# Kernel tuning notes

Measured on AMD Instinct MI355X. Metric: run time of the kernel, lower is better.

## Reference

```python
import jax, jax.numpy as jnp
import numpy as np
from jax import lax

DIM = 512


def rmsnorm(x, gamma):
    # F.normalize(x, dim=-1) * sqrt(dim) * (gamma + 1)
    n = jnp.maximum(jnp.linalg.norm(x, axis=-1, keepdims=True), 1e-12)
    return x / n * (DIM ** 0.5) * (gamma + 1.0)


def lru_layer(x, Wn, Wif, Whf, bhf):
    # x: [b, t, d]. Precompute the input-dependent projections as big matmuls,
    # then scan the genuinely sequential hidden recurrence.
    nh = jnp.tanh(jnp.einsum('btd,de->bte', x, Wn))   # candidate hidden
    ifg = jnp.einsum('btd,de->bte', x, Wif)            # input forget logits
    b = x.shape[0]
    h0 = jnp.zeros((b, DIM), dtype=x.dtype)            # init_hidden buffer (zeros)

    def step(h, inp):
        nh_t, if_t = inp                               # [b, d] each
        g = jax.nn.sigmoid(h @ Whf + bhf + if_t)       # forget gate
        h_next = h + g * (nh_t - h)                    # lerp(h, nh, g)
        return h_next, h_next

    _, hs = lax.scan(step, h0, (jnp.swapaxes(nh, 0, 1), jnp.swapaxes(ifg, 0, 1)))
    return jnp.swapaxes(hs, 0, 1)                      # [b, t, d]


def gate_cell(x, hidden, Wn, Wif, Whf, bhf):
    # LightRecurrentUnitCell applied pointwise over [b, t, d] with hidden=x_in
    nh = jnp.tanh(jnp.einsum('btd,de->bte', x, Wn))
    g = jax.nn.sigmoid(jnp.einsum('btd,de->bte', hidden, Whf) + bhf
                       + jnp.einsum('btd,de->bte', x, Wif))
    return hidden + g * (nh - hidden)


def setup_inputs() -> dict:
    key = jax.random.key(0)
    ks = jax.random.split(key, 12)
    s = 1.0 / np.sqrt(DIM)
    def w(k):
        return jax.random.uniform(k, (DIM, DIM), jnp.float32, -s, s)
    inp = {
        'x': jax.random.normal(ks[0], (32, 2048, DIM), jnp.float32),
        'gamma': jnp.zeros((DIM,), jnp.float32),
        'g_Wn': w(ks[1]), 'g_Wif': w(ks[2]), 'g_Whf': w(ks[3]),
        'g_bhf': jax.random.uniform(ks[4], (DIM,), jnp.float32, -s, s),
        'l0_Wn': w(ks[5]), 'l0_Wif': w(ks[6]), 'l0_Whf': w(ks[7]),
        'l0_bhf': jax.random.uniform(ks[8], (DIM,), jnp.float32, -s, s),
        'l1_Wn': w(ks[9]), 'l1_Wif': w(ks[10]), 'l1_Whf': w(ks[11]),
        'l1_bhf': jax.random.uniform(jax.random.fold_in(key, 99), (DIM,), jnp.float32, -s, s),
    }
    return inp


def reference(x, gamma, g_Wn, g_Wif, g_Whf, g_bhf,
              l0_Wn, l0_Wif, l0_Whf, l0_bhf,
              l1_Wn, l1_Wif, l1_Whf, l1_bhf):
    xn = rmsnorm(x, gamma)
    h = lru_layer(xn, l0_Wn, l0_Wif, l0_Whf, l0_bhf)
    h = lru_layer(h, l1_Wn, l1_Wif, l1_Whf, l1_bhf)
    lru_out = gate_cell(h, xn, g_Wn, g_Wif, g_Whf, g_bhf)
    return lru_out + x
```

## Files before the change

### kernel.cpp

```cpp
#include <hip/hip_runtime.h>
#include <stdint.h>

#define D 512
#define BATCH 32
#define TT 2048
#define BT (BATCH*TT)

typedef unsigned short u16;
typedef __attribute__((ext_vector_type(8))) short bf16x8;
typedef __attribute__((ext_vector_type(4))) float f32x4;

__device__ __forceinline__ float bf2f(u16 u){
  union { unsigned int i; float f; } v; v.i = ((unsigned int)u) << 16; return v.f;
}
__device__ __forceinline__ u16 f2bf(float f){
  union { float f; unsigned int i; } v; v.f = f;
  unsigned int r = (v.i + 0x7fffu + ((v.i >> 16) & 1u)) >> 16;
  return (u16)r;
}

__device__ __forceinline__ int dot4i8(int a, int b, int c){
#if __has_builtin(__builtin_amdgcn_sdot4)
  return __builtin_amdgcn_sdot4(a, b, c, false);
#else
  c += (int)(char)(a      ) * (int)(char)(b      );
  c += (int)(char)(a >>  8) * (int)(char)(b >>  8);
  c += (int)(char)(a >> 16) * (int)(char)(b >> 16);
  c += (int)(char)(a >> 24) * (int)(char)(b >> 24);
  return c;
#endif
}

__global__ __launch_bounds__(256) void rmsnorm_k(const float* __restrict__ x,
                                                 const float* __restrict__ gamma,
                                                 u16* __restrict__ xn){
  int row = blockIdx.x;
  int t = threadIdx.x;
  const float* xr = x + (size_t)row * D;
  float v0 = xr[t];
  float v1 = xr[t + 256];
  float s = v0*v0 + v1*v1;
  #pragma unroll
  for (int o = 32; o > 0; o >>= 1) s += __shfl_down(s, o);
  __shared__ float red[4];
  int lane = t & 63, wv = t >> 6;
  if (lane == 0) red[wv] = s;
  __syncthreads();
  float tot = red[0] + red[1] + red[2] + red[3];
  float n = fmaxf(sqrtf(tot), 1e-12f);
  float sc = 22.627416997969522f / n;
  u16* o_ = xn + (size_t)row * D;
  o_[t]       = f2bf(v0 * sc * (gamma[t] + 1.f));
  o_[t + 256] = f2bf(v1 * sc * (gamma[t + 256] + 1.f));
}

__global__ __launch_bounds__(256) void transpose_k(const float* __restrict__ src,
                                                   u16* __restrict__ dst){
  __shared__ u16 tile[32][33];
  int bx = blockIdx.x * 32, by = blockIdx.y * 32;
  int tx = threadIdx.x & 31, ty = threadIdx.x >> 5;
  #pragma unroll
  for (int i = 0; i < 32; i += 8)
    tile[ty + i][tx] = f2bf(src[(size_t)(by + ty + i) * D + bx + tx]);
  __syncthreads();
  #pragma unroll
  for (int i = 0; i < 32; i += 8)
    dst[(size_t)(bx + ty + i) * D + by + tx] = tile[tx][ty + i];
}

__global__ __launch_bounds__(64) void quant_col_k(const float* __restrict__ W,
                                                  int* __restrict__ Wq,
                                                  float* __restrict__ sc){
  int e = blockIdx.x;
  int lane = threadIdx.x;
  float w[8];
  float m = 0.f;
  #pragma unroll
  for (int j = 0; j < 8; j++){
    w[j] = W[(size_t)(lane*8 + j) * D + e];
    m = fmaxf(m, fabsf(w[j]));
  }
  #pragma unroll
  for (int o = 32; o > 0; o >>= 1) m = fmaxf(m, __shfl_xor(m, o));
  float inv = (m > 0.f) ? (127.f / m) : 0.f;
  int q[8];
  #pragma unroll
  for (int j = 0; j < 8; j++){
    int v = __float2int_rn(w[j] * inv);
    v = v < -127 ? -127 : (v > 127 ? 127 : v);
    q[j] = v & 0xff;
  }
  int p0 = q[0] | (q[1] << 8) | (q[2] << 16) | (q[3] << 24);
  int p1 = q[4] | (q[5] << 8) | (q[6] << 16) | (q[7] << 24);
  Wq[e*128 + lane*2]     = p0;
  Wq[e*128 + lane*2 + 1] = p1;
  if (lane == 0) sc[e] = m / (127.f * 127.f);
}

__global__ __launch_bounds__(256) void gemm_bt_k(const u16* __restrict__ A,
                                                 const u16* __restrict__ Bt,
                                                 u16* __restrict__ C,
                                                 int do_tanh){
  __shared__ __align__(16) u16 As[128*32];
  __shared__ __align__(16) u16 Bs[128*32];
  int tid = threadIdx.x;
  int bm = blockIdx.x, bn = blockIdx.y;
  int wv = tid >> 6, lane = tid & 63;
  int wm = (wv & 1) * 64, wn = (wv >> 1) * 64;
  int m0 = lane & 15, quad = lane >> 4;
  f32x4 acc[4][4];
  #pragma unroll
  for (int i = 0; i < 4; i++)
    #pragma unroll
    for (int j = 0; j < 4; j++){
      f32x4 z = {0.f, 0.f, 0.f, 0.f};
      acc[i][j] = z;
    }
  const size_t arow = (size_t)bm * 128;
  const size_t brow = (size_t)bn * 128;
  for (int k0 = 0; k0 < D; k0 += 32){
    __syncthreads();
    #pragma unroll
    for (int i = 0; i < 2; i++){
      int c = tid + 256*i;
      int r = c >> 2, ko = (c & 3) * 8;
      ((int4*)As)[c] = *(const int4*)(A  + (arow + r) * D + k0 + ko);
      ((int4*)Bs)[c] = *(const int4*)(Bt + (brow + r) * D + k0 + ko);
    }
    __syncthreads();
    bf16x8 af[4], bfr[4];
    #pragma unroll
    for (int i = 0; i < 4; i++){
      af[i]  = *(const bf16x8*)(As + (wm + i*16 + m0) * 32 + quad*8);
      bfr[i] = *(const bf16x8*)(Bs + (wn + i*16 + m0) * 32 + quad*8);
    }
    #pragma unroll
    for (int i = 0; i < 4; i++)
      #pragma unroll
      for (int j = 0; j < 4; j++)
        acc[i][j] = __builtin_amdgcn_mfma_f32_16x16x32_bf16(af[i], bfr[j], acc[i][j], 0, 0, 0);
  }
  #pragma unroll
  for (int i = 0; i < 4; i++)
    #pragma unroll
    for (int j = 0; j < 4; j++)
      #pragma unroll
      for (int r = 0; r < 4; r++){
        size_t row = arow + wm + i*16 + quad*4 + r;
        int col = bn*128 + wn + j*16 + m0;
        float v = acc[i][j][r];
        if (do_tanh) v = tanhf(v);
        C[row * D + col] = f2bf(v);
      }
}

__global__ __launch_bounds__(512, 2) void lru_scan_k(u16* __restrict__ Nn,
                                                     const u16* __restrict__ Ff,
                                                     const int* __restrict__ Wq,
                                                     const float* __restrict__ sc,
                                                     const float* __restrict__ bhf){
  int tid = threadIdx.x;
  int b = blockIdx.x;
  int wv = tid >> 6, l = tid & 63;
  int m  = l & 15;
  int q2 = l >> 4;
  int base_e = wv*64 + m*4;
  int e = base_e + q2;

  int4 wq[4][8];
  #pragma unroll
  for (int j = 0; j < 4; j++){
    const int* wp = Wq + (size_t)(base_e + j) * 128 + q2*32;
    #pragma unroll
    for (int i = 0; i < 8; i++) wq[j][i] = ((const int4*)wp)[i];
  }
  float scale = sc[e];
  float bias  = bhf[e];

  __shared__ __align__(16) char hq[2][512];
  if (tid < 128) ((int*)hq[0])[tid] = 0;
  float h = 0.f;
  const size_t base = (size_t)b * TT * D + e;
  u16* np = Nn + base;
  const u16* fp = Ff + base;
  float nv  = bf2f(np[0]);
  float fvb = bf2f(fp[0]) + bias;
  __syncthreads();

  for (int t = 0; t < TT; t++){
    float nv_n = 0.f, fvb_n = 0.f;
    if (t < TT - 1){
      nv_n  = bf2f(np[(size_t)(t+1) * D]);
      fvb_n = bf2f(fp[(size_t)(t+1) * D]) + bias;
    }
    const char* hb = hq[t & 1] + q2*128;
    int p0 = 0, p1 = 0, p2 = 0, p3 = 0;
    #pragma unroll
    for (int i = 0; i < 8; i++){
      int4 a = ((const int4*)hb)[i];
      p0 = dot4i8(wq[0][i].x, a.x, p0); p0 = dot4i8(wq[0][i].y, a.y, p0);
      p0 = dot4i8(wq[0][i].z, a.z, p0); p0 = dot4i8(wq[0][i].w, a.w, p0);
      p1 = dot4i8(wq[1][i].x, a.x, p1); p1 = dot4i8(wq[1][i].y, a.y, p1);
      p1 = dot4i8(wq[1][i].z, a.z, p1); p1 = dot4i8(wq[1][i].w, a.w, p1);
      p2 = dot4i8(wq[2][i].x, a.x, p2); p2 = dot4i8(wq[2][i].y, a.y, p2);
      p2 = dot4i8(wq[2][i].z, a.z, p2); p2 = dot4i8(wq[2][i].w, a.w, p2);
      p3 = dot4i8(wq[3][i].x, a.x, p3); p3 = dot4i8(wq[3][i].y, a.y, p3);
      p3 = dot4i8(wq[3][i].z, a.z, p3); p3 = dot4i8(wq[3][i].w, a.w, p3);
    }
    int b0 = q2 & 1, b1 = q2 >> 1;
    int send0 = b0 ? p0 : p1, keep0 = b0 ? p1 : p0;
    int send1 = b0 ? p2 : p3, keep1 = b0 ? p3 : p2;
    int z0 = keep0 + __shfl_xor(send0, 16);
    int z1 = keep1 + __shfl_xor(send1, 16);
    int zs = b1 ? z0 : z1, zk = b1 ? z1 : z0;
    int z  = zk + __shfl_xor(zs, 32);
    float arg = (float)z * scale + fvb;
    float g = 1.f / (1.f + __expf(-arg));
    h = h + g * (nv - h);
    np[(size_t)t * D] = f2bf(h);
    int q = __float2int_rn(h * 127.f);
    q = q < -127 ? -127 : (q > 127 ? 127 : q);
    hq[(t+1) & 1][e] = (char)q;
    nv = nv_n; fvb = fvb_n;
    asm volatile("s_waitcnt lgkmcnt(0)\n\ts_barrier" ::: "memory");
  }
}

__global__ __launch_bounds__(256) void final1_k(const u16* __restrict__ xn,
                                                u16* __restrict__ Nng,
                                                const u16* __restrict__ Ffg,
                                                const u16* __restrict__ Ghf,
                                                const float* __restrict__ gbhf){
  size_t i = (size_t)blockIdx.x * 256 + threadIdx.x;
  int e = (int)(i & (D - 1));
  float xnv = bf2f(xn[i]);
  float nv  = bf2f(Nng[i]);
  float arg = bf2f(Ghf[i]) + gbhf[e] + bf2f(Ffg[i]);
  float g = 1.f / (1.f + __expf(-arg));
  float lru = xnv + g * (nv - xnv);
  Nng[i] = f2bf(lru);
}

__global__ __launch_bounds__(256) void final2_k(const u16* __restrict__ lru,
                                                const float* __restrict__ x,
                                                float* __restrict__ out){
  size_t i = (size_t)blockIdx.x * 256 + threadIdx.x;
  out[i] = bf2f(lru[i]) + x[i];
}

extern "C" void kernel_launch(void* const* d_in, const int* in_sizes, int n_in,
                              void* d_out, int out_size, void* d_ws, size_t ws_size,
                              hipStream_t stream){
  const float* x      = (const float*)d_in[0];
  const float* gamma  = (const float*)d_in[1];
  const float* g_Wn   = (const float*)d_in[2];
  const float* g_Wif  = (const float*)d_in[3];
  const float* g_Whf  = (const float*)d_in[4];
  const float* g_bhf  = (const float*)d_in[5];
  const float* l0_Wn  = (const float*)d_in[6];
  const float* l0_Wif = (const float*)d_in[7];
  const float* l0_Whf = (const float*)d_in[8];
  const float* l0_bhf = (const float*)d_in[9];
  const float* l1_Wn  = (const float*)d_in[10];
  const float* l1_Wif = (const float*)d_in[11];
  const float* l1_Whf = (const float*)d_in[12];
  const float* l1_bhf = (const float*)d_in[13];
  float* out = (float*)d_out;

  char* ws = (char*)d_ws;
  const size_t PLANE = (size_t)BT * D * 2;
  u16* P0 = (u16*)(ws);
  u16* P1 = (u16*)(ws + PLANE);
  u16* P2 = (u16*)d_out;
  u16* P3 = P2 + (size_t)BT * D;

  char* wb = ws + 2*PLANE;
  const size_t WSZ = (size_t)D * D * 2;
  u16* T_l0Wn  = (u16*)(wb + 0*WSZ);
  u16* T_l0Wif = (u16*)(wb + 1*WSZ);
  u16* T_gWhf  = (u16*)(wb + 2*WSZ);
  u16* T_l1Wn  = (u16*)(wb + 3*WSZ);
  u16* T_l1Wif = (u16*)(wb + 4*WSZ);
  u16* T_gWn   = (u16*)(wb + 5*WSZ);
  u16* T_gWif  = (u16*)(wb + 6*WSZ);
  int*   Wq0 = (int*)  (wb + 7*WSZ);
  int*   Wq1 = (int*)  (wb + 7*WSZ + (size_t)D*D);
  float* sc0 = (float*)(wb + 7*WSZ + 2*(size_t)D*D);
  float* sc1 = (float*)(wb + 7*WSZ + 2*(size_t)D*D + D*4);

  dim3 tb(256), tg(16, 16);
  transpose_k<<<tg, tb, 0, stream>>>(l0_Wn,  T_l0Wn);
  transpose_k<<<tg, tb, 0, stream>>>(l0_Wif, T_l0Wif);
  transpose_k<<<tg, tb, 0, stream>>>(g_Whf,  T_gWhf);
  transpose_k<<<tg, tb, 0, stream>>>(l1_Wn,  T_l1Wn);
  transpose_k<<<tg, tb, 0, stream>>>(l1_Wif, T_l1Wif);
  transpose_k<<<tg, tb, 0, stream>>>(g_Wn,   T_gWn);
  transpose_k<<<tg, tb, 0, stream>>>(g_Wif,  T_gWif);
  quant_col_k<<<512, 64, 0, stream>>>(l0_Whf, Wq0, sc0);
  quant_col_k<<<512, 64, 0, stream>>>(l1_Whf, Wq1, sc1);

  rmsnorm_k<<<BT, 256, 0, stream>>>(x, gamma, P0);

  dim3 gg(BT/128, D/128);
  gemm_bt_k<<<gg, tb, 0, stream>>>(P0, T_l0Wn,  P1, 1);
  gemm_bt_k<<<gg, tb, 0, stream>>>(P0, T_l0Wif, P2, 0);
  lru_scan_k<<<BATCH, 512, 0, stream>>>(P1, P2, Wq0, sc0, l0_bhf);
  gemm_bt_k<<<gg, tb, 0, stream>>>(P1, T_l1Wn,  P3, 1);
  gemm_bt_k<<<gg, tb, 0, stream>>>(P1, T_l1Wif, P2, 0);
  lru_scan_k<<<BATCH, 512, 0, stream>>>(P3, P2, Wq1, sc1, l1_bhf);
  gemm_bt_k<<<gg, tb, 0, stream>>>(P3, T_gWn,  P1, 1);
  gemm_bt_k<<<gg, tb, 0, stream>>>(P3, T_gWif, P2, 0);
  gemm_bt_k<<<gg, tb, 0, stream>>>(P0, T_gWhf, P3, 0);

  final1_k<<<BT*D/256, 256, 0, stream>>>(P0, P1, P2, P3, g_bhf);
  final2_k<<<BT*D/256, 256, 0, stream>>>(P1, x, out);
}
```

Measured before the change: 4.195 ms.

## Fuse both LRU scans and middle GEMMs into one pipelined persistent kernel

Replaces the layer-0 scan, the two layer-1 projection GEMMs and the layer-1 scan with one 96-block kernel. Blocks 0-31 run the layer-0 scan and publish progress flags every 64 timesteps. Blocks 32-63 compute the layer-1 projections per 64-row chunk as soon as it is ready, and blocks 64-95 run the layer-1 scan behind them. The goal is to overlap the two sequential scans and the GEMM so the second scan no longer waits for the first to finish. In exchange it relies on all 96 blocks being co-resident, since it spin-waits on flags with a bounded timeout. The projection blocks also read weights straight from global memory with less reuse than the tiled GEMM.

```diff
diff --git a/kernel.cpp b/kernel.cpp
--- a/kernel.cpp
+++ b/kernel.cpp
@@ -29,6 +29,15 @@
   c += (int)(char)(a >> 24) * (int)(char)(b >> 24);
   return c;
 #endif
+}
+
+__device__ __forceinline__ void spin_wait_ge(const int* p, int target){
+  int iters = 0;
+  while (__hip_atomic_load(p, __ATOMIC_RELAXED, __HIP_MEMORY_SCOPE_AGENT) < target){
+    __builtin_amdgcn_s_sleep(16);
+    if (++iters > 4000000) break;
+  }
+  __builtin_amdgcn_fence(__ATOMIC_ACQUIRE, "agent");
 }
 
 __global__ __launch_bounds__(256) void rmsnorm_k(const float* __restrict__ x,
@@ -154,13 +163,13 @@
       }
 }
 
-__global__ __launch_bounds__(512, 2) void lru_scan_k(u16* __restrict__ Nn,
-                                                     const u16* __restrict__ Ff,
-                                                     const int* __restrict__ Wq,
-                                                     const float* __restrict__ sc,
-                                                     const float* __restrict__ bhf){
-  int tid = threadIdx.x;
-  int b = blockIdx.x;
+__device__ __forceinline__ void scan_core(u16* __restrict__ Nn,
+                                          const u16* __restrict__ Ff,
+                                          const int* __restrict__ Wq,
+                                          const float* __restrict__ sc,
+                                          const float* __restrict__ bhf,
+                                          int b, int tid, char* smem,
+                                          int* prog_pub, const int* prog_wait){
   int wv = tid >> 6, l = tid & 63;
   int m  = l & 15;
   int q2 = l >> 4;
@@ -177,17 +186,23 @@
   float scale = sc[e];
   float bias  = bhf[e];
 
-  __shared__ __align__(16) char hq[2][512];
-  if (tid < 128) ((int*)hq[0])[tid] = 0;
+  char (*hq)[512] = (char(*)[512])smem;
+  if (tid < 128) ((int*)smem)[tid] = 0;
   float h = 0.f;
   const size_t base = (size_t)b * TT * D + e;
   u16* np = Nn + base;
   const u16* fp = Ff + base;
+
+  if (prog_wait) spin_wait_ge(prog_wait + b, 128);
   float nv  = bf2f(np[0]);
   float fvb = bf2f(fp[0]) + bias;
   __syncthreads();
 
   for (int t = 0; t < TT; t++){
+    if (prog_wait && t && (t & 63) == 0){
+      int target = t + 128; if (target > TT) target = TT;
+      spin_wait_ge(prog_wait + b, target);
+    }
     float nv_n = 0.f, fvb_n = 0.f;
     if (t < TT - 1){
       nv_n  = bf2f(np[(size_t)(t+1) * D]);
@@ -223,7 +238,106 @@
     hq[(t+1) & 1][e] = (char)q;
     nv = nv_n; fvb = fvb_n;
     asm volatile("s_waitcnt lgkmcnt(0)\n\ts_barrier" ::: "memory");
-  }
+    if (prog_pub && (t & 63) == 63){
+      asm volatile("s_waitcnt vmcnt(0)" ::: "memory");
+      __syncthreads();
+      if (tid == 0)
+        __hip_atomic_store(prog_pub + b, t + 1, __ATOMIC_RELEASE,
+                           __HIP_MEMORY_SCOPE_AGENT);
+    }
+  }
+}
+
+#define LDA 260
+__global__ __launch_bounds__(512, 1) void fused_mid_k(
+    u16* __restrict__ P1,
+    const u16* __restrict__ P2,
+    u16* __restrict__ P3,
+    const u16* __restrict__ Wn1t, const u16* __restrict__ Wif1t,
+    const int* __restrict__ Wq0, const float* __restrict__ sc0,
+    const float* __restrict__ bhf0,
+    const int* __restrict__ Wq1, const float* __restrict__ sc1,
+    const float* __restrict__ bhf1,
+    int* __restrict__ prog0, int* __restrict__ prog1){
+  __shared__ __align__(16) char smem[64 * LDA * 2];
+  int blk = blockIdx.x, tid = threadIdx.x;
+
+  if (blk < 32){
+    scan_core(P1, P2, Wq0, sc0, bhf0, blk, tid, smem, prog0, nullptr);
+  } else if (blk < 64){
+    int b = blk - 32;
+    u16* As = (u16*)smem;
+    const size_t bbase = (size_t)b * TT * D;
+    int wv = tid >> 6, lane = tid & 63;
+    int m0 = lane & 15, quad = lane >> 4;
+    int wn = wv * 64;
+    for (int c = 0; c < TT/64; c++){
+      int r0 = c * 64;
+      spin_wait_ge(prog0 + b, r0 + 64);
+      f32x4 accA[4][4], accB[4][4];
+      #pragma unroll
+      for (int i = 0; i < 4; i++)
+        #pragma unroll
+        for (int j = 0; j < 4; j++){
+          f32x4 zz = {0.f, 0.f, 0.f, 0.f};
+          accA[i][j] = zz; accB[i][j] = zz;
+        }
+      for (int kh = 0; kh < 2; kh++){
+        __syncthreads();
+        #pragma unroll
+        for (int j = 0; j < 4; j++){
+          int idx = tid + 512*j;
+          int row = idx >> 5, k8 = idx & 31;
+          *(int4*)(As + row*LDA + k8*8) =
+            *(const int4*)(P1 + bbase + (size_t)(r0 + row)*D + kh*256 + k8*8);
+        }
+        __syncthreads();
+        #pragma unroll
+        for (int ks = 0; ks < 8; ks++){
+          int k0g = kh*256 + ks*32, k0l = ks*32;
+          bf16x8 af[4], bA[4], bB[4];
+          #pragma unroll
+          for (int i = 0; i < 4; i++)
+            af[i] = *(const bf16x8*)(As + (i*16 + m0)*LDA + k0l + quad*8);
+          #pragma unroll
+          for (int j = 0; j < 4; j++){
+            size_t n = (size_t)(wn + j*16 + m0);
+            bA[j] = *(const bf16x8*)(Wn1t  + n*D + k0g + quad*8);
+            bB[j] = *(const bf16x8*)(Wif1t + n*D + k0g + quad*8);
+          }
+          #pragma unroll
+          for (int i = 0; i < 4; i++)
+            #pragma unroll
+            for (int j = 0; j < 4; j++){
+              accA[i][j] = __builtin_amdgcn_mfma_f32_16x16x32_bf16(af[i], bA[j], accA[i][j], 0, 0, 0);
+              accB[i][j] = __builtin_amdgcn_mfma_f32_16x16x32_bf16(af[i], bB[j], accB[i][j], 0, 0, 0);
+            }
+        }
+      }
+      #pragma unroll
+      for (int i = 0; i < 4; i++)
+        #pragma unroll
+        for (int j = 0; j < 4; j++)
+          #pragma unroll
+          for (int r = 0; r < 4; r++){
+            size_t row = (size_t)(r0 + i*16 + quad*4 + r);
+            int col = wn + j*16 + m0;
+            P3[bbase + row*D + col] = f2bf(tanhf(accA[i][j][r]));
+            P1[bbase + row*D + col] = f2bf(accB[i][j][r]);
+          }
+      asm volatile("s_waitcnt vmcnt(0)" ::: "memory");
+      __syncthreads();
+      if (tid == 0)
+        __hip_atomic_store(prog1 + b, r0 + 64, __ATOMIC_RELEASE,
+                           __HIP_MEMORY_SCOPE_AGENT);
+    }
+  } else {
+    scan_core(P3, P1, Wq1, sc1, bhf1, blk - 64, tid, smem, nullptr, prog1);
+  }
+}
+
+__global__ __launch_bounds__(64) void zero_flags_k(int* __restrict__ f){
+  f[threadIdx.x] = 0;
 }
 
 __global__ __launch_bounds__(256) void final1_k(const u16* __restrict__ xn,
@@ -287,6 +401,7 @@
   int*   Wq1 = (int*)  (wb + 7*WSZ + (size_t)D*D);
   float* sc0 = (float*)(wb + 7*WSZ + 2*(size_t)D*D);
   float* sc1 = (float*)(wb + 7*WSZ + 2*(size_t)D*D + D*4);
+  int*  prog = (int*)  (wb + 7*WSZ + 2*(size_t)D*D + 2*D*4);
 
   dim3 tb(256), tg(16, 16);
   transpose_k<<<tg, tb, 0, stream>>>(l0_Wn,  T_l0Wn);
@@ -298,16 +413,16 @@
   transpose_k<<<tg, tb, 0, stream>>>(g_Wif,  T_gWif);
   quant_col_k<<<512, 64, 0, stream>>>(l0_Whf, Wq0, sc0);
   quant_col_k<<<512, 64, 0, stream>>>(l1_Whf, Wq1, sc1);
+  zero_flags_k<<<1, 64, 0, stream>>>(prog);
 
   rmsnorm_k<<<BT, 256, 0, stream>>>(x, gamma, P0);
 
   dim3 gg(BT/128, D/128);
   gemm_bt_k<<<gg, tb, 0, stream>>>(P0, T_l0Wn,  P1, 1);
   gemm_bt_k<<<gg, tb, 0, stream>>>(P0, T_l0Wif, P2, 0);
-  lru_scan_k<<<BATCH, 512, 0, stream>>>(P1, P2, Wq0, sc0, l0_bhf);
-  gemm_bt_k<<<gg, tb, 0, stream>>>(P1, T_l1Wn,  P3, 1);
-  gemm_bt_k<<<gg, tb, 0, stream>>>(P1, T_l1Wif, P2, 0);
-  lru_scan_k<<<BATCH, 512, 0, stream>>>(P3, P2, Wq1, sc1, l1_bhf);
+  fused_mid_k<<<96, 512, 0, stream>>>(P1, P2, P3, T_l1Wn, T_l1Wif,
+                                      Wq0, sc0, l0_bhf, Wq1, sc1, l1_bhf,
+                                      prog, prog + 32);
   gemm_bt_k<<<gg, tb, 0, stream>>>(P3, T_gWn,  P1, 1);
   gemm_bt_k<<<gg, tb, 0, stream>>>(P3, T_gWif, P2, 0);
   gemm_bt_k<<<gg, tb, 0, stream>>>(P0, T_gWhf, P3, 0);
```

After: 3.435 ms. 1.22x faster.
